# Kernel tuning notes

Measured on AMD Instinct MI355X. Metric: run time of the kernel, lower is better.

Reference implementation:

```python
import jax, jax.numpy as jnp
import numpy as np

N_QUBIT = 4  # kernel_size 2*2
PI = np.pi


def _rx(a):
    c = jnp.cos(a / 2).astype(jnp.complex64)
    s = jnp.sin(a / 2).astype(jnp.complex64)
    js = 1j * s
    return jnp.stack([jnp.stack([c, -js], -1), jnp.stack([-js, c], -1)], -2)


def _ry(a):
    c = jnp.cos(a / 2).astype(jnp.complex64)
    s = jnp.sin(a / 2).astype(jnp.complex64)
    return jnp.stack([jnp.stack([c, -s], -1), jnp.stack([s, c], -1)], -2)


def _rz(a):
    ac = a.astype(jnp.complex64) if hasattr(a, 'astype') else jnp.asarray(a, jnp.complex64)
    e = jnp.exp(-0.5j * ac)
    f = jnp.exp(0.5j * ac)
    z = jnp.zeros_like(e)
    return jnp.stack([jnp.stack([e, z], -1), jnp.stack([z, f], -1)], -2)


def _apply_1q(psi, U, qubit):
    # psi: [N, 2,2,2,2]; U: [N,2,2] (per-line gate) or [2,2] (shared gate)
    axis = 1 + qubit
    psi = jnp.moveaxis(psi, axis, -1)
    if U.ndim == 3:
        psi = jnp.einsum('nab,n...b->n...a', U, psi)
    else:
        psi = jnp.einsum('ab,...b->...a', U, psi)
    return jnp.moveaxis(psi, -1, axis)


def _cz_mask(c, t):
    # CZ is diagonal: flip sign of amplitudes with both bits 1 (same math as the 4x4 tensordot)
    m = np.ones((2, 2), np.complex64)
    m[1, 1] = -1
    shape = [1] * N_QUBIT
    shape[c] = 2
    shape[t] = 2
    return jnp.asarray(m.reshape(shape))


def setup_inputs() -> dict:
    key = jax.random.key(0)
    k1, k2 = jax.random.split(key)
    x = jax.random.uniform(k1, (128, 2048, N_QUBIT, 3), dtype=jnp.float32)
    w = jax.random.normal(k2, (2, N_QUBIT, 3), dtype=jnp.float32)
    return {"x": x, "w": w}


def reference(x, w):
    B, L, nq, _ = x.shape
    N = B * L
    lines = x.reshape(N, nq, 3)
    # |0...0> state
    psi = jnp.zeros((N,) + (2,) * nq, jnp.complex64)
    psi = psi.at[(slice(None),) + (0,) * nq].set(1.0 + 0.0j)
    # angle-encoding: RZ(pi*x0) RY(pi*x1) RZ(pi*x2) per qubit
    for n in range(nq):
        psi = _apply_1q(psi, _rz(PI * lines[:, n, 0]), n)
        psi = _apply_1q(psi, _ry(PI * lines[:, n, 1]), n)
        psi = _apply_1q(psi, _rz(PI * lines[:, n, 2]), n)
    n_layer = w.shape[0]
    for h in range(n_layer):
        for i in range(nq):
            psi = _apply_1q(psi, _rx(w[h, i, 0]), i)
            psi = _apply_1q(psi, _ry(w[h, i, 1]), i)
            psi = _apply_1q(psi, _rz(w[h, i, 2]), i)
        for ie in range(1, nq, 2):
            psi = psi * _cz_mask(ie - 1, ie)[None]
        for ie in range(2, nq, 2):
            psi = psi * _cz_mask(ie - 1, ie)[None]
    # PauliZ expectation per qubit: sum(prob | bit=0) - sum(prob | bit=1)
    prob = psi.real ** 2 + psi.imag ** 2  # [N,2,2,2,2] float32
    zvals = []
    for i in range(nq):
        p = jnp.moveaxis(prob, 1 + i, 1).reshape(N, 2, -1).sum(-1)
        zvals.append(p[:, 0] - p[:, 1])
    return jnp.stack(zvals, -1).reshape(B, L, nq)
```

## Files before the change

kernel.cpp:

```cpp
#include <hip/hip_runtime.h>

#define PI_F 3.14159265358979323846f

__device__ __forceinline__ float2 cmul(float2 a, float2 b) {
    return make_float2(fmaf(a.x, b.x, -a.y * b.y), fmaf(a.x, b.y, a.y * b.x));
}
__device__ __forceinline__ float2 cadd(float2 a, float2 b) {
    return make_float2(a.x + b.x, a.y + b.y);
}
__device__ __forceinline__ void mm2(const float2 A[2][2], const float2 B[2][2], float2 C[2][2]) {
    #pragma unroll
    for (int i = 0; i < 2; ++i)
        #pragma unroll
        for (int j = 0; j < 2; ++j)
            C[i][j] = cadd(cmul(A[i][0], B[0][j]), cmul(A[i][1], B[1][j]));
}

__global__ __launch_bounds__(256) void qcnn_kernel(const float* __restrict__ x,
                                                   const float* __restrict__ w,
                                                   float* __restrict__ out,
                                                   int N) {
    __shared__ float2 Ush[2][4][4];
    const int t = threadIdx.x;
    if (t < 8) {
        const int h = t >> 2, q = t & 3;
        const float a = 0.5f * w[(h * 4 + q) * 3 + 0];
        const float b = 0.5f * w[(h * 4 + q) * 3 + 1];
        const float c = 0.5f * w[(h * 4 + q) * 3 + 2];
        const float ca = __cosf(a), sa = __sinf(a);
        const float cb = __cosf(b), sb = __sinf(b);
        const float cc = __cosf(c), sc = __sinf(c);
        float2 RX[2][2] = {{{ca, 0.f}, {0.f, -sa}}, {{0.f, -sa}, {ca, 0.f}}};
        float2 RY[2][2] = {{{cb, 0.f}, {-sb, 0.f}}, {{sb, 0.f}, {cb, 0.f}}};
        float2 RZ[2][2] = {{{cc, -sc}, {0.f, 0.f}}, {{0.f, 0.f}, {cc, sc}}};
        float2 T[2][2], U[2][2];
        mm2(RY, RX, T);
        mm2(RZ, T, U);
        Ush[h][q][0] = U[0][0];
        Ush[h][q][1] = U[0][1];
        Ush[h][q][2] = U[1][0];
        Ush[h][q][3] = U[1][1];
    }
    __syncthreads();

    const int n = blockIdx.x * blockDim.x + threadIdx.x;
    if (n >= N) return;

    const float4* xv = (const float4*)(x + (size_t)n * 12);
    const float4 xa = xv[0], xb = xv[1], xc = xv[2];
    const float xy[4] = {xa.y, xb.x, xb.w, xc.z};
    const float xz[4] = {xa.z, xb.y, xc.x, xc.w};

    float2 v[4][2];
    #pragma unroll
    for (int q = 0; q < 4; ++q) {
        const float ty = 0.5f * PI_F * xy[q];
        const float tz = 0.5f * PI_F * xz[q];
        const float cy = __cosf(ty), sy = __sinf(ty);
        const float cz = __cosf(tz), sz = __sinf(tz);
        v[q][0] = make_float2(cy * cz, -cy * sz);
        v[q][1] = make_float2(sy * cz, sy * sz);
    }

    float2 t01[4], t23[4], psi[16];
    #pragma unroll
    for (int i = 0; i < 2; ++i)
        #pragma unroll
        for (int j = 0; j < 2; ++j) {
            t01[i * 2 + j] = cmul(v[0][i], v[1][j]);
            t23[i * 2 + j] = cmul(v[2][i], v[3][j]);
        }
    #pragma unroll
    for (int i = 0; i < 4; ++i)
        #pragma unroll
        for (int j = 0; j < 4; ++j)
            psi[i * 4 + j] = cmul(t01[i], t23[j]);

    const unsigned czmask = (1u << 3) | (1u << 6) | (1u << 11) |
                            (1u << 12) | (1u << 13) | (1u << 15);

    #pragma unroll
    for (int h = 0; h < 2; ++h) {
        #pragma unroll
        for (int q = 0; q < 4; ++q) {
            const float2 U00 = Ush[h][q][0], U01 = Ush[h][q][1];
            const float2 U10 = Ush[h][q][2], U11 = Ush[h][q][3];
            const int stride = 8 >> q;
            #pragma unroll
            for (int k = 0; k < 8; ++k) {
                const int lo = k & (stride - 1);
                const int i0 = ((k - lo) << 1) | lo;
                const int i1 = i0 | stride;
                const float2 p0 = psi[i0], p1 = psi[i1];
                psi[i0] = cadd(cmul(U00, p0), cmul(U01, p1));
                psi[i1] = cadd(cmul(U10, p0), cmul(U11, p1));
            }
        }
        #pragma unroll
        for (int idx = 0; idx < 16; ++idx)
            if ((czmask >> idx) & 1) {
                psi[idx].x = -psi[idx].x;
                psi[idx].y = -psi[idx].y;
            }
    }

    float z[4] = {0.f, 0.f, 0.f, 0.f};
    #pragma unroll
    for (int idx = 0; idx < 16; ++idx) {
        const float p = fmaf(psi[idx].x, psi[idx].x, psi[idx].y * psi[idx].y);
        #pragma unroll
        for (int q = 0; q < 4; ++q)
            z[q] += ((idx >> (3 - q)) & 1) ? -p : p;
    }
    ((float4*)out)[n] = make_float4(z[0], z[1], z[2], z[3]);
}

extern "C" void kernel_launch(void* const* d_in, const int* in_sizes, int n_in,
                              void* d_out, int out_size, void* d_ws, size_t ws_size,
                              hipStream_t stream) {
    const float* x = (const float*)d_in[0];
    const float* w = (const float*)d_in[1];
    float* out = (float*)d_out;
    const int N = in_sizes[0] / 12;
    const int block = 256;
    const int grid = (N + block - 1) / block;
    qcnn_kernel<<<grid, block, 0, stream>>>(x, w, out, N);
}
```

Baseline: 68.86 us.

## Replace statevector simulation with closed-form Bloch-vector expectation formulas

The kernel no longer builds and evolves a 16-amplitude statevector. It represents each qubit as a Bloch vector, rotates it with a precomputed 3x3 rotation from the first layer, and evaluates the final Z expectations analytically, using the CZ-chain structure to multiply in the neighbours' z components. A separate tiny kernel precomputes the rotation coefficients into the workspace, replacing the per-block shared-memory setup and sync. This removes most of the arithmetic per line, leaving the kernel bound mainly by memory traffic. It adds a second launch and relies on the derived formula being exact for this two-layer, four-qubit circuit; the final layer's RZ is dropped because it commutes with the Z measurement.

Measured after the change: 63.68 us. 1.08x faster.

```diff
diff --git a/kernel.cpp b/kernel.cpp
--- a/kernel.cpp
+++ b/kernel.cpp
@@ -1,48 +1,45 @@
 #include <hip/hip_runtime.h>
+#include <math.h>
 
 #define PI_F 3.14159265358979323846f
 
-__device__ __forceinline__ float2 cmul(float2 a, float2 b) {
-    return make_float2(fmaf(a.x, b.x, -a.y * b.y), fmaf(a.x, b.y, a.y * b.x));
-}
-__device__ __forceinline__ float2 cadd(float2 a, float2 b) {
-    return make_float2(a.x + b.x, a.y + b.y);
-}
-__device__ __forceinline__ void mm2(const float2 A[2][2], const float2 B[2][2], float2 C[2][2]) {
-    #pragma unroll
-    for (int i = 0; i < 2; ++i)
-        #pragma unroll
-        for (int j = 0; j < 2; ++j)
-            C[i][j] = cadd(cmul(A[i][0], B[0][j]), cmul(A[i][1], B[1][j]));
+
+__global__ void qcnn_precompute(const float* __restrict__ w, float* __restrict__ ws) {
+    const int q = threadIdx.x;
+    if (q >= 4) return;
+    {
+        const float a = w[q * 3 + 0], b = w[q * 3 + 1], c = w[q * 3 + 2];
+        float sa, ca, sb, cb, sc, cc;
+        sincosf(a, &sa, &ca);
+        sincosf(b, &sb, &cb);
+        sincosf(c, &sc, &cc);
+        float* o = ws + q * 12;
+        o[0] = cc * cb;
+        o[1] = cc * sb * sa - sc * ca;
+        o[2] = cc * sb * ca + sc * sa;
+        o[3] = sc * cb;
+        o[4] = sc * sb * sa + cc * ca;
+        o[5] = sc * sb * ca - cc * sa;
+        o[6] = -sb;
+        o[7] = cb * sa;
+        o[8] = cb * ca;
+    }
+    {
+        const float a = w[12 + q * 3 + 0], b = w[12 + q * 3 + 1];
+        float sa, ca, sb, cb;
+        sincosf(a, &sa, &ca);
+        sincosf(b, &sb, &cb);
+        float* o = ws + q * 12;
+        o[9] = -sb;
+        o[10] = cb * sa;
+        o[11] = cb * ca;
+    }
 }
 
 __global__ __launch_bounds__(256) void qcnn_kernel(const float* __restrict__ x,
-                                                   const float* __restrict__ w,
+                                                   const float* __restrict__ cw,
                                                    float* __restrict__ out,
                                                    int N) {
-    __shared__ float2 Ush[2][4][4];
-    const int t = threadIdx.x;
-    if (t < 8) {
-        const int h = t >> 2, q = t & 3;
-        const float a = 0.5f * w[(h * 4 + q) * 3 + 0];
-        const float b = 0.5f * w[(h * 4 + q) * 3 + 1];
-        const float c = 0.5f * w[(h * 4 + q) * 3 + 2];
-        const float ca = __cosf(a), sa = __sinf(a);
-        const float cb = __cosf(b), sb = __sinf(b);
-        const float cc = __cosf(c), sc = __sinf(c);
-        float2 RX[2][2] = {{{ca, 0.f}, {0.f, -sa}}, {{0.f, -sa}, {ca, 0.f}}};
-        float2 RY[2][2] = {{{cb, 0.f}, {-sb, 0.f}}, {{sb, 0.f}, {cb, 0.f}}};
-        float2 RZ[2][2] = {{{cc, -sc}, {0.f, 0.f}}, {{0.f, 0.f}, {cc, sc}}};
-        float2 T[2][2], U[2][2];
-        mm2(RY, RX, T);
-        mm2(RZ, T, U);
-        Ush[h][q][0] = U[0][0];
-        Ush[h][q][1] = U[0][1];
-        Ush[h][q][2] = U[1][0];
-        Ush[h][q][3] = U[1][1];
-    }
-    __syncthreads();
-
     const int n = blockIdx.x * blockDim.x + threadIdx.x;
     if (n >= N) return;
 
@@ -51,67 +48,32 @@
     const float xy[4] = {xa.y, xb.x, xb.w, xc.z};
     const float xz[4] = {xa.z, xb.y, xc.x, xc.w};
 
-    float2 v[4][2];
+    float px[4], py[4], pz[4];
     #pragma unroll
     for (int q = 0; q < 4; ++q) {
-        const float ty = 0.5f * PI_F * xy[q];
-        const float tz = 0.5f * PI_F * xz[q];
-        const float cy = __cosf(ty), sy = __sinf(ty);
-        const float cz = __cosf(tz), sz = __sinf(tz);
-        v[q][0] = make_float2(cy * cz, -cy * sz);
-        v[q][1] = make_float2(sy * cz, sy * sz);
+        float st, ct, sp, cp;
+        __sincosf(PI_F * xy[q], &st, &ct);
+        __sincosf(PI_F * xz[q], &sp, &cp);
+        const float mx = st * cp, my = st * sp, mz = ct;
+        const float* M = cw + q * 12;
+        px[q] = fmaf(M[0], mx, fmaf(M[1], my, M[2] * mz));
+        py[q] = fmaf(M[3], mx, fmaf(M[4], my, M[5] * mz));
+        pz[q] = fmaf(M[6], mx, fmaf(M[7], my, M[8] * mz));
     }
 
-    float2 t01[4], t23[4], psi[16];
+    float z[4];
     #pragma unroll
-    for (int i = 0; i < 2; ++i)
-        #pragma unroll
-        for (int j = 0; j < 2; ++j) {
-            t01[i * 2 + j] = cmul(v[0][i], v[1][j]);
-            t23[i * 2 + j] = cmul(v[2][i], v[3][j]);
-        }
-    #pragma unroll
-    for (int i = 0; i < 4; ++i)
-        #pragma unroll
-        for (int j = 0; j < 4; ++j)
-            psi[i * 4 + j] = cmul(t01[i], t23[j]);
-
-    const unsigned czmask = (1u << 3) | (1u << 6) | (1u << 11) |
-                            (1u << 12) | (1u << 13) | (1u << 15);
-
-    #pragma unroll
-    for (int h = 0; h < 2; ++h) {
-        #pragma unroll
-        for (int q = 0; q < 4; ++q) {
-            const float2 U00 = Ush[h][q][0], U01 = Ush[h][q][1];
-            const float2 U10 = Ush[h][q][2], U11 = Ush[h][q][3];
-            const int stride = 8 >> q;
-            #pragma unroll
-            for (int k = 0; k < 8; ++k) {
-                const int lo = k & (stride - 1);
-                const int i0 = ((k - lo) << 1) | lo;
-                const int i1 = i0 | stride;
-                const float2 p0 = psi[i0], p1 = psi[i1];
-                psi[i0] = cadd(cmul(U00, p0), cmul(U01, p1));
-                psi[i1] = cadd(cmul(U10, p0), cmul(U11, p1));
-            }
-        }
-        #pragma unroll
-        for (int idx = 0; idx < 16; ++idx)
-            if ((czmask >> idx) & 1) {
-                psi[idx].x = -psi[idx].x;
-                psi[idx].y = -psi[idx].y;
-            }
+    for (int q = 0; q < 4; ++q) {
+        const float* M = cw + q * 12;
+        const float xyterm = fmaf(M[9], px[q], M[10] * py[q]);
+        float nb;
+        if (q == 0) nb = pz[1];
+        else if (q == 1) nb = pz[0] * pz[2];
+        else if (q == 2) nb = pz[1] * pz[3];
+        else nb = pz[2];
+        z[q] = fmaf(M[11], pz[q], xyterm * nb);
     }
 
-    float z[4] = {0.f, 0.f, 0.f, 0.f};
-    #pragma unroll
-    for (int idx = 0; idx < 16; ++idx) {
-        const float p = fmaf(psi[idx].x, psi[idx].x, psi[idx].y * psi[idx].y);
-        #pragma unroll
-        for (int q = 0; q < 4; ++q)
-            z[q] += ((idx >> (3 - q)) & 1) ? -p : p;
-    }
     ((float4*)out)[n] = make_float4(z[0], z[1], z[2], z[3]);
 }
 
@@ -121,8 +83,12 @@
     const float* x = (const float*)d_in[0];
     const float* w = (const float*)d_in[1];
     float* out = (float*)d_out;
+    float* ws = (float*)d_ws;
     const int N = in_sizes[0] / 12;
+
+    qcnn_precompute<<<1, 64, 0, stream>>>(w, ws);
+
     const int block = 256;
     const int grid = (N + block - 1) / block;
-    qcnn_kernel<<<grid, block, 0, stream>>>(x, w, out, N);
+    qcnn_kernel<<<grid, block, 0, stream>>>(x, ws, out, N);
 }
```
